# Performance work log

Measured on AMD Instinct MI355X. Metric: run time of the kernel, lower is better.

Reference implementation:

```python
import jax, jax.numpy as jnp
import numpy as np

H = 64   # LSTM hidden size
NL = 8   # LSTM layers
B, T = 2048, 64


def setup_inputs() -> dict:
    key = jax.random.key(0)
    ks = jax.random.split(key, 18)
    r = lambda i, shape, s=0.1: jax.random.normal(ks[i], shape, dtype=jnp.float32) * s
    return {
        "x": r(0, (B, T, 2), 1.0),
        "w1": r(1, (16, 2)), "b1": r(2, (16,)),
        "w2": r(3, (16, 16)), "b2": r(4, (16,)),
        "w_ih0": r(5, (4 * H, 16)), "w_hh0": r(6, (4 * H, H)),
        "b_ih0": r(7, (4 * H,)), "b_hh0": r(8, (4 * H,)),
        "w_ih": r(9, (NL - 1, 4 * H, H)), "w_hh": r(10, (NL - 1, 4 * H, H)),
        "b_ih": r(11, (NL - 1, 4 * H)), "b_hh": r(12, (NL - 1, 4 * H)),
        "wo1": r(13, (32, H)), "bo1": r(14, (32,)),
        "wo2": r(15, (4, 32)), "bo2": r(16, (4,)),
    }


def _lstm_layer(x, w_ih, w_hh, b):
    # x: [B, T, I]; torch gate order: i, f, g, o
    bsz = x.shape[0]
    xg = jnp.einsum('bti,gi->btg', x, w_ih) + b  # [B, T, 4H] precomputed input gates

    def step(carry, xg_t):
        h, c = carry
        gates = xg_t + h @ w_hh.T
        i, f, g, o = jnp.split(gates, 4, axis=-1)
        i = jax.nn.sigmoid(i); f = jax.nn.sigmoid(f)
        g = jnp.tanh(g); o = jax.nn.sigmoid(o)
        c = f * c + i * g
        h = o * jnp.tanh(c)
        return (h, c), h

    h0 = jnp.zeros((bsz, H), x.dtype)
    _, hs = jax.lax.scan(step, (h0, h0), jnp.swapaxes(xg, 0, 1))  # [T, B, H]
    return jnp.swapaxes(hs, 0, 1)


def reference(x, w1, b1, w2, b2, w_ih0, w_hh0, b_ih0, b_hh0,
              w_ih, w_hh, b_ih, b_hh, wo1, bo1, wo2, bo2):
    # action-input MLP: 2 -> 16 -> relu -> 16
    h = jax.nn.relu(x @ w1.T + b1) @ w2.T + b2
    # 8-layer LSTM, hidden 64
    h = _lstm_layer(h, w_ih0, w_hh0, b_ih0 + b_hh0)
    for l in range(NL - 1):
        h = _lstm_layer(h, w_ih[l], w_hh[l], b_ih[l] + b_hh[l])
    # output MLP: 64 -> 32 -> relu -> 4
    return jax.nn.relu(h @ wo1.T + bo1) @ wo2.T + bo2
```

## Files before the change

### kernel.cpp

```cpp
#include <hip/hip_runtime.h>


#define BATCH 2048
#define TT 64
#define HH 64
#define RS 72

typedef short bf16x8 __attribute__((ext_vector_type(8)));
typedef float f32x4 __attribute__((ext_vector_type(4)));

__device__ __forceinline__ float sigmoid_fast(float x) {
    return __builtin_amdgcn_rcpf(1.f + __expf(-x));
}
__device__ __forceinline__ float tanh_fast(float x) {
    float e = __expf(-2.f * x);
    e = fminf(e, 1e30f);
    return (1.f - e) * __builtin_amdgcn_rcpf(1.f + e);
}
__device__ __forceinline__ void split2(float x, unsigned short& hi, unsigned short& lo) {
    const unsigned u = __float_as_uint(x);
    hi = (unsigned short)(u >> 16);
    const float r = x - __uint_as_float(u & 0xFFFF0000u);
    lo = (unsigned short)(__float_as_uint(r) >> 16);
}
__device__ __forceinline__ unsigned short bf16_rne(float x) {
    const unsigned u = __float_as_uint(x);
    return (unsigned short)((u + 0x7FFFu + ((u >> 16) & 1u)) >> 16);
}
__device__ __forceinline__ void wg_wait(int* c, int v) {
    while (__hip_atomic_load(c, __ATOMIC_ACQUIRE, __HIP_MEMORY_SCOPE_WORKGROUP) < v) {}
}
__device__ __forceinline__ void wg_bump(int* c, int lane) {
    if (lane == 0)
        __hip_atomic_fetch_add(c, 1, __ATOMIC_RELEASE, __HIP_MEMORY_SCOPE_WORKGROUP);
}

__global__ __launch_bounds__(256)
void mlp_in_kernel(const float* __restrict__ x,
                   const float* __restrict__ w1, const float* __restrict__ b1,
                   const float* __restrict__ w2, const float* __restrict__ b2,
                   float* __restrict__ out) {
    const int gid = blockIdx.x * 256 + threadIdx.x;
    const float x0 = x[gid * 2 + 0];
    const float x1 = x[gid * 2 + 1];
    float hid[16];
#pragma unroll
    for (int j = 0; j < 16; ++j) {
        float v = fmaf(x1, w1[j * 2 + 1], fmaf(x0, w1[j * 2 + 0], b1[j]));
        hid[j] = fmaxf(0.f, v);
    }
    float o[16];
#pragma unroll
    for (int oo = 0; oo < 16; ++oo) {
        float acc = b2[oo];
#pragma unroll
        for (int j = 0; j < 16; ++j) acc = fmaf(hid[j], w2[oo * 16 + j], acc);
        o[oo] = acc;
    }
    float4* op = (float4*)(out + gid * 16);
#pragma unroll
    for (int q = 0; q < 4; ++q) {
        float4 v;
        v.x = o[q * 4 + 0]; v.y = o[q * 4 + 1]; v.z = o[q * 4 + 2]; v.w = o[q * 4 + 3];
        op[q] = v;
    }
}

template <int IA, int IPADA>
__global__ __launch_bounds__(512, 2)
void lstm_pair(const float* __restrict__ xmlp,
               unsigned* __restrict__ P,
               float* __restrict__ houtf,
               const int last,
               const float* __restrict__ wihA, const float* __restrict__ whhA,
               const float* __restrict__ biA, const float* __restrict__ bhA,
               const float* __restrict__ wihB, const float* __restrict__ whhB,
               const float* __restrict__ biB, const float* __restrict__ bhB) {
    constexpr int KTA = (IPADA + 64) / 32;
    constexpr int KTX = IPADA / 32;
    constexpr int LDPA = IPADA + 8;
    __shared__ __align__(16) unsigned short pAh[2][16 * LDPA], pAl[2][16 * LDPA];
    __shared__ __align__(16) unsigned short rHh[4][16 * RS], rHl[4][16 * RS];
    __shared__ __align__(16) unsigned short pHh[2][16 * RS], pHl[2][16 * RS];
    __shared__ int cA, cB, cBm;

    const int tid = threadIdx.x;
    const int wv = tid >> 6, lane = tid & 63, l16 = lane & 15, quad = lane >> 4;
    const int grp = wv >> 2;
    const int wg = wv & 3;
    const int base = blockIdx.x * 8;
    const bool lo32 = (lane < 32);
    const int bpi = (lane & 31) << 2;

    if (tid == 0) { cA = 0; cB = 0; cBm = 0; }
    for (int e = tid; e < 2 * 16 * LDPA; e += 512) { (&pAh[0][0])[e] = 0; (&pAl[0][0])[e] = 0; }
    for (int e = tid; e < 4 * 16 * RS; e += 512)   { (&rHh[0][0])[e] = 0; (&rHl[0][0])[e] = 0; }
    for (int e = tid; e < 2 * 16 * RS; e += 512)   { (&pHh[0][0])[e] = 0; (&pHl[0][0])[e] = 0; }

    const int I    = grp ? 64 : IA;
    const int IPAD = grp ? 64 : IPADA;
    const int KT   = grp ? 4  : KTA;
    const float* wih = grp ? wihB : wihA;
    const float* whh = grp ? whhB : whhA;
    const float* bi  = grp ? biB  : biA;
    const float* bh  = grp ? bhB  : bhA;

    const int jg = 16 * wg + l16;
    bf16x8 bhi[4][4];
    float bsum[4];
#pragma unroll
    for (int gt = 0; gt < 4; ++gt) {
        const int n = gt * 64 + jg;
        bsum[gt] = bi[n] + bh[n];
#pragma unroll
        for (int kt = 0; kt < 4; ++kt) {
            bf16x8 vh = {0, 0, 0, 0, 0, 0, 0, 0};
            if (kt < KT) {
#pragma unroll
                for (int j = 0; j < 8; ++j) {
                    const int k = kt * 32 + quad * 8 + j;
                    float w = 0.f;
                    if (k < I) w = wih[n * I + k];
                    else if (k >= IPAD) w = whh[n * 64 + (k - IPAD)];
                    vh[j] = (short)bf16_rne(w);
                }
            }
            bhi[kt][gt] = vh;
        }
    }

    float cs[2] = {0.f, 0.f};
    const int row0 = (quad & 1) * 4 + ((quad >> 1) << 1);

    float2 xr2 = {0.f, 0.f};
    uint2 xru = {0u, 0u};
    int sr = 0, sc = 0, srd = 0;
    bool stg = false;
    if (grp == 0) {
        if (IA == 16) {
            stg = (tid < 128);
            sr = tid >> 3; sc = (tid & 7) * 2;
            srd = base + (sr & 7);
            if (stg) {
                xr2 = *(const float2*)&xmlp[((size_t)srd * TT + 0) * 16 + sc];
                unsigned short h0, l0, h1, l1;
                split2(xr2.x, h0, l0); split2(xr2.y, h1, l1);
                *(unsigned*)&pAh[0][sr * LDPA + sc] = ((unsigned)h1 << 16) | h0;
                *(unsigned*)&pAl[0][sr * LDPA + sc] = ((unsigned)l1 << 16) | l0;
                xr2 = *(const float2*)&xmlp[((size_t)srd * TT + 1) * 16 + sc];
            }
        } else {
            stg = true;
            sr = tid >> 5; sc = (tid & 31) * 2;
            srd = base + sr;
            xru = *(const uint2*)&P[((size_t)srd * TT + 0) * 64 + sc];
            *(unsigned*)&pAh[0][sr * LDPA + sc] = (xru.y & 0xFFFF0000u) | (xru.x >> 16);
            *(unsigned*)&pAl[0][sr * LDPA + sc] = (xru.y << 16) | (xru.x & 0xFFFFu);
            xru = *(const uint2*)&P[((size_t)srd * TT + 1) * 64 + sc];
        }
    }
    __syncthreads();

    if (grp == 0) {
        __builtin_amdgcn_s_setprio(1);
        for (int t = 0; t < TT; ++t) {
            const int pb = t & 1;
            const int rsl = t & 3;
            const int rpr = (t + 3) & 3;
            if (t) wg_wait(&cA, 4 * t);
            if (stg) {
                if (IA == 16) {
                    unsigned short h0, l0, h1, l1;
                    split2(xr2.x, h0, l0); split2(xr2.y, h1, l1);
                    *(unsigned*)&pAh[pb ^ 1][sr * LDPA + sc] = ((unsigned)h1 << 16) | h0;
                    *(unsigned*)&pAl[pb ^ 1][sr * LDPA + sc] = ((unsigned)l1 << 16) | l0;
                    const int tp = (t + 2) & (TT - 1);
                    xr2 = *(const float2*)&xmlp[((size_t)srd * TT + tp) * 16 + sc];
                } else {
                    *(unsigned*)&pAh[pb ^ 1][sr * LDPA + sc] = (xru.y & 0xFFFF0000u) | (xru.x >> 16);
                    *(unsigned*)&pAl[pb ^ 1][sr * LDPA + sc] = (xru.y << 16) | (xru.x & 0xFFFFu);
                    const int tp = (t + 2) & (TT - 1);
                    xru = *(const uint2*)&P[((size_t)srd * TT + tp) * 64 + sc];
                }
            }
            bf16x8 ahi[4], alo[4];
#pragma unroll
            for (int kt = 0; kt < KTA; ++kt) {
                if (kt < KTX) {
                    const int aoff = l16 * LDPA + kt * 32 + quad * 8;
                    ahi[kt] = *(const bf16x8*)&pAh[pb][aoff];
                    alo[kt] = *(const bf16x8*)&pAl[pb][aoff];
                } else {
                    const int aoff = l16 * RS + (kt - KTX) * 32 + quad * 8;
                    ahi[kt] = *(const bf16x8*)&rHh[rpr][aoff];
                    alo[kt] = *(const bf16x8*)&rHl[rpr][aoff];
                }
            }
            f32x4 a0[4], a1[4];
#pragma unroll
            for (int gt = 0; gt < 4; ++gt) {
                a0[gt][0] = bsum[gt]; a0[gt][1] = bsum[gt];
                a0[gt][2] = bsum[gt]; a0[gt][3] = bsum[gt];
                a1[gt] = (f32x4){0.f, 0.f, 0.f, 0.f};
            }
            __builtin_amdgcn_s_setprio(2);
#pragma unroll
            for (int kt = 0; kt < KTA; ++kt) {
#pragma unroll
                for (int gt = 0; gt < 4; ++gt) {
                    a0[gt] = __builtin_amdgcn_mfma_f32_16x16x32_bf16(ahi[kt], bhi[kt][gt], a0[gt], 0, 0, 0);
                    a1[gt] = __builtin_amdgcn_mfma_f32_16x16x32_bf16(alo[kt], bhi[kt][gt], a1[gt], 0, 0, 0);
                }
            }
            __builtin_amdgcn_s_setprio(1);
            f32x4 s4[4];
#pragma unroll
            for (int gt = 0; gt < 4; ++gt) s4[gt] = a0[gt] + a1[gt];
            float gk[4][2];
#pragma unroll
            for (int gt = 0; gt < 4; ++gt) {
#pragma unroll
                for (int r = 0; r < 2; ++r) {
                    const float up = __uint_as_float(
                        __builtin_amdgcn_ds_bpermute(bpi, __float_as_uint(s4[gt][r + 2])));
                    gk[gt][r] = lo32 ? s4[gt][r] : up;
                }
            }
            float hv[2];
#pragma unroll
            for (int r = 0; r < 2; ++r) {
                const float iv = sigmoid_fast(gk[0][r]);
                const float fv = sigmoid_fast(gk[1][r]);
                const float gv = tanh_fast(gk[2][r]);
                const float ov = sigmoid_fast(gk[3][r]);
                const float cn = fv * cs[r] + iv * gv;
                cs[r] = cn;
                hv[r] = ov * tanh_fast(cn);
            }
            if (t >= 4) wg_wait(&cBm, 4 * (t - 3));
#pragma unroll
            for (int r = 0; r < 2; ++r) {
                const int R = row0 + r;
                unsigned short h_, l_;
                split2(hv[r], h_, l_);
                rHh[rsl][R * RS + jg] = h_;
                rHl[rsl][R * RS + jg] = l_;
            }
            wg_bump(&cA, lane);
        }
    } else {
        for (int t = 0; t < TT; ++t) {
            const int pb = t & 1;
            const int rsl = t & 3;
            if (t) wg_wait(&cB, 4 * t);
            wg_wait(&cA, 4 * (t + 1));
            bf16x8 ahi[4], alo[4];
#pragma unroll
            for (int kt = 0; kt < 2; ++kt) {
                const int aoff = l16 * RS + kt * 32 + quad * 8;
                ahi[kt] = *(const bf16x8*)&rHh[rsl][aoff];
                alo[kt] = *(const bf16x8*)&rHl[rsl][aoff];
            }
#pragma unroll
            for (int kt = 2; kt < 4; ++kt) {
                const int aoff = l16 * RS + (kt - 2) * 32 + quad * 8;
                ahi[kt] = *(const bf16x8*)&pHh[pb ^ 1][aoff];
                alo[kt] = *(const bf16x8*)&pHl[pb ^ 1][aoff];
            }
            wg_bump(&cBm, lane);
            f32x4 a0[4], a1[4];
#pragma unroll
            for (int gt = 0; gt < 4; ++gt) {
                a0[gt][0] = bsum[gt]; a0[gt][1] = bsum[gt];
                a0[gt][2] = bsum[gt]; a0[gt][3] = bsum[gt];
                a1[gt] = (f32x4){0.f, 0.f, 0.f, 0.f};
            }
            __builtin_amdgcn_s_setprio(1);
#pragma unroll
            for (int kt = 0; kt < 4; ++kt) {
#pragma unroll
                for (int gt = 0; gt < 4; ++gt) {
                    a0[gt] = __builtin_amdgcn_mfma_f32_16x16x32_bf16(ahi[kt], bhi[kt][gt], a0[gt], 0, 0, 0);
                    a1[gt] = __builtin_amdgcn_mfma_f32_16x16x32_bf16(alo[kt], bhi[kt][gt], a1[gt], 0, 0, 0);
                }
            }
            __builtin_amdgcn_s_setprio(0);
            f32x4 s4[4];
#pragma unroll
            for (int gt = 0; gt < 4; ++gt) s4[gt] = a0[gt] + a1[gt];
            float gk[4][2];
#pragma unroll
            for (int gt = 0; gt < 4; ++gt) {
#pragma unroll
                for (int r = 0; r < 2; ++r) {
                    const float up = __uint_as_float(
                        __builtin_amdgcn_ds_bpermute(bpi, __float_as_uint(s4[gt][r + 2])));
                    gk[gt][r] = lo32 ? s4[gt][r] : up;
                }
            }
#pragma unroll
            for (int r = 0; r < 2; ++r) {
                const float iv = sigmoid_fast(gk[0][r]);
                const float fv = sigmoid_fast(gk[1][r]);
                const float gv = tanh_fast(gk[2][r]);
                const float ov = sigmoid_fast(gk[3][r]);
                const float cn = fv * cs[r] + iv * gv;
                cs[r] = cn;
                const float h = ov * tanh_fast(cn);
                const int R = row0 + r;
                unsigned short h_, l_;
                split2(h, h_, l_);
                pHh[pb][R * RS + jg] = h_;
                pHl[pb][R * RS + jg] = l_;
                if (!last) {
                    P[((size_t)(base + R) * TT + t) * 64 + jg] =
                        ((unsigned)h_ << 16) | (unsigned)l_;
                } else {
                    houtf[((size_t)(base + R) * TT + t) * HH + jg] = h;
                }
            }
            wg_bump(&cB, lane);
        }
    }
}

__global__ __launch_bounds__(256)
void mlp_out_kernel(const float* __restrict__ hin,
                    const float* __restrict__ wo1, const float* __restrict__ bo1,
                    const float* __restrict__ wo2, const float* __restrict__ bo2,
                    float* __restrict__ out) {
    __shared__ __align__(16) float wo1_s[32 * 64];
    __shared__ float bo1_s[32];
    __shared__ float wo2_s[4 * 32];
    __shared__ float bo2_s[4];
    const int tid = threadIdx.x;
    for (int e = tid; e < 32 * 64; e += 256) wo1_s[e] = wo1[e];
    if (tid < 32) bo1_s[tid] = bo1[tid];
    if (tid < 128) wo2_s[tid] = wo2[tid];
    if (tid < 4) bo2_s[tid] = bo2[tid];
    __syncthreads();

    const int gid = blockIdx.x * 256 + tid;
    const float4* hv = (const float4*)(hin + gid * 64);
    float4 h[16];
#pragma unroll
    for (int q = 0; q < 16; ++q) h[q] = hv[q];

    float m1[32];
#pragma unroll
    for (int o = 0; o < 32; ++o) {
        float acc = bo1_s[o];
        const float4* wrow = (const float4*)(wo1_s + o * 64);
#pragma unroll
        for (int q = 0; q < 16; ++q) {
            const float4 w = wrow[q];
            acc = fmaf(h[q].x, w.x, acc);
            acc = fmaf(h[q].y, w.y, acc);
            acc = fmaf(h[q].z, w.z, acc);
            acc = fmaf(h[q].w, w.w, acc);
        }
        m1[o] = fmaxf(0.f, acc);
    }
    float r[4];
#pragma unroll
    for (int q = 0; q < 4; ++q) {
        float acc = bo2_s[q];
#pragma unroll
        for (int o = 0; o < 32; ++o) acc = fmaf(m1[o], wo2_s[q * 32 + o], acc);
        r[q] = acc;
    }
    float4 res;
    res.x = r[0]; res.y = r[1]; res.z = r[2]; res.w = r[3];
    ((float4*)out)[gid] = res;
}

extern "C" void kernel_launch(void* const* d_in, const int* in_sizes, int n_in,
                              void* d_out, int out_size, void* d_ws, size_t ws_size,
                              hipStream_t stream) {
    const float* x     = (const float*)d_in[0];
    const float* w1    = (const float*)d_in[1];
    const float* b1    = (const float*)d_in[2];
    const float* w2    = (const float*)d_in[3];
    const float* b2    = (const float*)d_in[4];
    const float* w_ih0 = (const float*)d_in[5];
    const float* w_hh0 = (const float*)d_in[6];
    const float* b_ih0 = (const float*)d_in[7];
    const float* b_hh0 = (const float*)d_in[8];
    const float* w_ih  = (const float*)d_in[9];
    const float* w_hh  = (const float*)d_in[10];
    const float* b_ih  = (const float*)d_in[11];
    const float* b_hh  = (const float*)d_in[12];
    const float* wo1   = (const float*)d_in[13];
    const float* bo1   = (const float*)d_in[14];
    const float* wo2   = (const float*)d_in[15];
    const float* bo2   = (const float*)d_in[16];

    float* buf_mlp = (float*)d_ws;
    unsigned* P = (unsigned*)(buf_mlp + (size_t)BATCH * TT * 16);
    float* bufH = (float*)(P + (size_t)BATCH * TT * 64);

    const int nbt_blocks = (BATCH * TT) / 256;

    mlp_in_kernel<<<nbt_blocks, 256, 0, stream>>>(x, w1, b1, w2, b2, buf_mlp);

    lstm_pair<16, 32><<<BATCH / 8, 512, 0, stream>>>(
        buf_mlp, P, bufH, 0,
        w_ih0, w_hh0, b_ih0, b_hh0,
        w_ih + (size_t)0 * 256 * 64, w_hh + (size_t)0 * 256 * 64, b_ih + 0 * 256, b_hh + 0 * 256);

    for (int p = 1; p < 4; ++p) {
        const int la = 2 * p - 1, lb = 2 * p;
        lstm_pair<64, 64><<<BATCH / 8, 512, 0, stream>>>(
            buf_mlp, P, bufH, (p == 3) ? 1 : 0,
            w_ih + (size_t)la * 256 * 64, w_hh + (size_t)la * 256 * 64,
            b_ih + la * 256, b_hh + la * 256,
            w_ih + (size_t)lb * 256 * 64, w_hh + (size_t)lb * 256 * 64,
            b_ih + lb * 256, b_hh + lb * 256);
    }

    mlp_out_kernel<<<nbt_blocks, 256, 0, stream>>>(bufH, wo1, bo1, wo2, bo2, (float*)d_out);
}
```

Baseline: 478.2 us.

## Fuse four LSTM layers per kernel as a wavefront pipeline across wave groups

Replaces the two-layer-per-kernel pipeline (four launches) with a four-layer-per-block pipeline using 1024-thread blocks, so the 8 layers take two launches. Each group of four waves runs one layer and hands hidden states to the next group through LDS ring buffers, synchronised by per-layer counters. This halves the global round trips of intermediate activations and the pipeline fill/drain cost. In exchange it doubles block size and LDS use, and the launch bound of 4 may limit registers and occupancy, which could serialise more work per CU.

```diff
diff --git a/kernel.cpp b/kernel.cpp
--- a/kernel.cpp
+++ b/kernel.cpp
@@ -67,43 +67,47 @@
 }
 
 template <int IA, int IPADA>
-__global__ __launch_bounds__(512, 2)
-void lstm_pair(const float* __restrict__ xmlp,
-               unsigned* __restrict__ P,
+__global__ __launch_bounds__(1024, 4)
+void lstm_quad(const float* __restrict__ xmlp,
+               const unsigned* __restrict__ Pin,
+               unsigned* __restrict__ Pout,
                float* __restrict__ houtf,
-               const int last,
-               const float* __restrict__ wihA, const float* __restrict__ whhA,
-               const float* __restrict__ biA, const float* __restrict__ bhA,
-               const float* __restrict__ wihB, const float* __restrict__ whhB,
-               const float* __restrict__ biB, const float* __restrict__ bhB) {
+               const int p0, const int last,
+               const float* __restrict__ w_ih0, const float* __restrict__ w_hh0,
+               const float* __restrict__ b_ih0, const float* __restrict__ b_hh0,
+               const float* __restrict__ w_ih, const float* __restrict__ w_hh,
+               const float* __restrict__ b_ih, const float* __restrict__ b_hh) {
     constexpr int KTA = (IPADA + 64) / 32;
     constexpr int KTX = IPADA / 32;
     constexpr int LDPA = IPADA + 8;
     __shared__ __align__(16) unsigned short pAh[2][16 * LDPA], pAl[2][16 * LDPA];
-    __shared__ __align__(16) unsigned short rHh[4][16 * RS], rHl[4][16 * RS];
+    __shared__ __align__(16) unsigned short rh[3][4][16 * RS], rl[3][4][16 * RS];
     __shared__ __align__(16) unsigned short pHh[2][16 * RS], pHl[2][16 * RS];
-    __shared__ int cA, cB, cBm;
+    __shared__ int cc[4], mm[4];
 
     const int tid = threadIdx.x;
     const int wv = tid >> 6, lane = tid & 63, l16 = lane & 15, quad = lane >> 4;
-    const int grp = wv >> 2;
+    const int l = wv >> 2;
     const int wg = wv & 3;
     const int base = blockIdx.x * 8;
     const bool lo32 = (lane < 32);
     const int bpi = (lane & 31) << 2;
 
-    if (tid == 0) { cA = 0; cB = 0; cBm = 0; }
-    for (int e = tid; e < 2 * 16 * LDPA; e += 512) { (&pAh[0][0])[e] = 0; (&pAl[0][0])[e] = 0; }
-    for (int e = tid; e < 4 * 16 * RS; e += 512)   { (&rHh[0][0])[e] = 0; (&rHl[0][0])[e] = 0; }
-    for (int e = tid; e < 2 * 16 * RS; e += 512)   { (&pHh[0][0])[e] = 0; (&pHl[0][0])[e] = 0; }
-
-    const int I    = grp ? 64 : IA;
-    const int IPAD = grp ? 64 : IPADA;
-    const int KT   = grp ? 4  : KTA;
-    const float* wih = grp ? wihB : wihA;
-    const float* whh = grp ? whhB : whhA;
-    const float* bi  = grp ? biB  : biA;
-    const float* bh  = grp ? bhB  : bhA;
+    if (tid < 4) { cc[tid] = 0; mm[tid] = 0; }
+    for (int e = tid; e < 2 * 16 * LDPA; e += 1024) { (&pAh[0][0])[e] = 0; (&pAl[0][0])[e] = 0; }
+    for (int e = tid; e < 3 * 4 * 16 * RS; e += 1024) { (&rh[0][0][0])[e] = 0; (&rl[0][0][0])[e] = 0; }
+    for (int e = tid; e < 2 * 16 * RS; e += 1024) { (&pHh[0][0])[e] = 0; (&pHl[0][0])[e] = 0; }
+
+    const int L = p0 + l;
+    const float *wih, *whh, *bi, *bh;
+    int I, IPAD, KT;
+    if (L == 0) { wih = w_ih0; whh = w_hh0; bi = b_ih0; bh = b_hh0; I = IA; IPAD = IPADA; KT = KTA; }
+    else {
+        const int li = L - 1;
+        wih = w_ih + (size_t)li * 256 * 64; whh = w_hh + (size_t)li * 256 * 64;
+        bi = b_ih + li * 256; bh = b_hh + li * 256;
+        I = 64; IPAD = 64; KT = 4;
+    }
 
     const int jg = 16 * wg + l16;
     bf16x8 bhi[4][4];
@@ -136,7 +140,7 @@
     uint2 xru = {0u, 0u};
     int sr = 0, sc = 0, srd = 0;
     bool stg = false;
-    if (grp == 0) {
+    if (l == 0 && wv < 4) {
         if (IA == 16) {
             stg = (tid < 128);
             sr = tid >> 3; sc = (tid & 7) * 2;
@@ -150,24 +154,25 @@
                 xr2 = *(const float2*)&xmlp[((size_t)srd * TT + 1) * 16 + sc];
             }
         } else {
-            stg = true;
+            stg = (tid < 256);
             sr = tid >> 5; sc = (tid & 31) * 2;
             srd = base + sr;
-            xru = *(const uint2*)&P[((size_t)srd * TT + 0) * 64 + sc];
-            *(unsigned*)&pAh[0][sr * LDPA + sc] = (xru.y & 0xFFFF0000u) | (xru.x >> 16);
-            *(unsigned*)&pAl[0][sr * LDPA + sc] = (xru.y << 16) | (xru.x & 0xFFFFu);
-            xru = *(const uint2*)&P[((size_t)srd * TT + 1) * 64 + sc];
+            if (stg) {
+                xru = *(const uint2*)&Pin[((size_t)srd * TT + 0) * 64 + sc];
+                *(unsigned*)&pAh[0][sr * LDPA + sc] = (xru.y & 0xFFFF0000u) | (xru.x >> 16);
+                *(unsigned*)&pAl[0][sr * LDPA + sc] = (xru.y << 16) | (xru.x & 0xFFFFu);
+                xru = *(const uint2*)&Pin[((size_t)srd * TT + 1) * 64 + sc];
+            }
         }
     }
     __syncthreads();
 
-    if (grp == 0) {
+    if (l == 0) {
         __builtin_amdgcn_s_setprio(1);
         for (int t = 0; t < TT; ++t) {
             const int pb = t & 1;
-            const int rsl = t & 3;
-            const int rpr = (t + 3) & 3;
-            if (t) wg_wait(&cA, 4 * t);
+            const int rsl = t & 3, rpr = (t + 3) & 3;
+            if (t) wg_wait(&cc[0], 4 * t);
             if (stg) {
                 if (IA == 16) {
                     unsigned short h0, l0, h1, l1;
@@ -180,7 +185,7 @@
                     *(unsigned*)&pAh[pb ^ 1][sr * LDPA + sc] = (xru.y & 0xFFFF0000u) | (xru.x >> 16);
                     *(unsigned*)&pAl[pb ^ 1][sr * LDPA + sc] = (xru.y << 16) | (xru.x & 0xFFFFu);
                     const int tp = (t + 2) & (TT - 1);
-                    xru = *(const uint2*)&P[((size_t)srd * TT + tp) * 64 + sc];
+                    xru = *(const uint2*)&Pin[((size_t)srd * TT + tp) * 64 + sc];
                 }
             }
             bf16x8 ahi[4], alo[4];
@@ -192,8 +197,8 @@
                     alo[kt] = *(const bf16x8*)&pAl[pb][aoff];
                 } else {
                     const int aoff = l16 * RS + (kt - KTX) * 32 + quad * 8;
-                    ahi[kt] = *(const bf16x8*)&rHh[rpr][aoff];
-                    alo[kt] = *(const bf16x8*)&rHl[rpr][aoff];
+                    ahi[kt] = *(const bf16x8*)&rh[0][rpr][aoff];
+                    alo[kt] = *(const bf16x8*)&rl[0][rpr][aoff];
                 }
             }
             f32x4 a0[4], a1[4];
@@ -237,37 +242,108 @@
                 cs[r] = cn;
                 hv[r] = ov * tanh_fast(cn);
             }
-            if (t >= 4) wg_wait(&cBm, 4 * (t - 3));
+            if (t >= 4) wg_wait(&mm[1], 4 * (t - 3));
 #pragma unroll
             for (int r = 0; r < 2; ++r) {
                 const int R = row0 + r;
                 unsigned short h_, l_;
                 split2(hv[r], h_, l_);
-                rHh[rsl][R * RS + jg] = h_;
-                rHl[rsl][R * RS + jg] = l_;
-            }
-            wg_bump(&cA, lane);
+                rh[0][rsl][R * RS + jg] = h_;
+                rl[0][rsl][R * RS + jg] = l_;
+            }
+            wg_bump(&cc[0], lane);
+        }
+    } else if (l < 3) {
+        for (int t = 0; t < TT; ++t) {
+            const int rsl = t & 3, rpr = (t + 3) & 3;
+            if (t) wg_wait(&cc[l], 4 * t);
+            wg_wait(&cc[l - 1], 4 * (t + 1));
+            bf16x8 ahi[4], alo[4];
+#pragma unroll
+            for (int kt = 0; kt < 2; ++kt) {
+                const int aoff = l16 * RS + kt * 32 + quad * 8;
+                ahi[kt] = *(const bf16x8*)&rh[l - 1][rsl][aoff];
+                alo[kt] = *(const bf16x8*)&rl[l - 1][rsl][aoff];
+            }
+            wg_bump(&mm[l], lane);
+#pragma unroll
+            for (int kt = 2; kt < 4; ++kt) {
+                const int aoff = l16 * RS + (kt - 2) * 32 + quad * 8;
+                ahi[kt] = *(const bf16x8*)&rh[l][rpr][aoff];
+                alo[kt] = *(const bf16x8*)&rl[l][rpr][aoff];
+            }
+            f32x4 a0[4], a1[4];
+#pragma unroll
+            for (int gt = 0; gt < 4; ++gt) {
+                a0[gt][0] = bsum[gt]; a0[gt][1] = bsum[gt];
+                a0[gt][2] = bsum[gt]; a0[gt][3] = bsum[gt];
+                a1[gt] = (f32x4){0.f, 0.f, 0.f, 0.f};
+            }
+            __builtin_amdgcn_s_setprio(1);
+#pragma unroll
+            for (int kt = 0; kt < 4; ++kt) {
+#pragma unroll
+                for (int gt = 0; gt < 4; ++gt) {
+                    a0[gt] = __builtin_amdgcn_mfma_f32_16x16x32_bf16(ahi[kt], bhi[kt][gt], a0[gt], 0, 0, 0);
+                    a1[gt] = __builtin_amdgcn_mfma_f32_16x16x32_bf16(alo[kt], bhi[kt][gt], a1[gt], 0, 0, 0);
+                }
+            }
+            __builtin_amdgcn_s_setprio(0);
+            f32x4 s4[4];
+#pragma unroll
+            for (int gt = 0; gt < 4; ++gt) s4[gt] = a0[gt] + a1[gt];
+            float gk[4][2];
+#pragma unroll
+            for (int gt = 0; gt < 4; ++gt) {
+#pragma unroll
+                for (int r = 0; r < 2; ++r) {
+                    const float up = __uint_as_float(
+                        __builtin_amdgcn_ds_bpermute(bpi, __float_as_uint(s4[gt][r + 2])));
+                    gk[gt][r] = lo32 ? s4[gt][r] : up;
+                }
+            }
+            float hv[2];
+#pragma unroll
+            for (int r = 0; r < 2; ++r) {
+                const float iv = sigmoid_fast(gk[0][r]);
+                const float fv = sigmoid_fast(gk[1][r]);
+                const float gv = tanh_fast(gk[2][r]);
+                const float ov = sigmoid_fast(gk[3][r]);
+                const float cn = fv * cs[r] + iv * gv;
+                cs[r] = cn;
+                hv[r] = ov * tanh_fast(cn);
+            }
+            if (t >= 4) wg_wait(&mm[l + 1], 4 * (t - 3));
+#pragma unroll
+            for (int r = 0; r < 2; ++r) {
+                const int R = row0 + r;
+                unsigned short h_, l_;
+                split2(hv[r], h_, l_);
+                rh[l][rsl][R * RS + jg] = h_;
+                rl[l][rsl][R * RS + jg] = l_;
+            }
+            wg_bump(&cc[l], lane);
         }
     } else {
         for (int t = 0; t < TT; ++t) {
             const int pb = t & 1;
             const int rsl = t & 3;
-            if (t) wg_wait(&cB, 4 * t);
-            wg_wait(&cA, 4 * (t + 1));
+            if (t) wg_wait(&cc[3], 4 * t);
+            wg_wait(&cc[2], 4 * (t + 1));
             bf16x8 ahi[4], alo[4];
 #pragma unroll
             for (int kt = 0; kt < 2; ++kt) {
                 const int aoff = l16 * RS + kt * 32 + quad * 8;
-                ahi[kt] = *(const bf16x8*)&rHh[rsl][aoff];
-                alo[kt] = *(const bf16x8*)&rHl[rsl][aoff];
-            }
+                ahi[kt] = *(const bf16x8*)&rh[2][rsl][aoff];
+                alo[kt] = *(const bf16x8*)&rl[2][rsl][aoff];
+            }
+            wg_bump(&mm[3], lane);
 #pragma unroll
             for (int kt = 2; kt < 4; ++kt) {
                 const int aoff = l16 * RS + (kt - 2) * 32 + quad * 8;
                 ahi[kt] = *(const bf16x8*)&pHh[pb ^ 1][aoff];
                 alo[kt] = *(const bf16x8*)&pHl[pb ^ 1][aoff];
             }
-            wg_bump(&cBm, lane);
             f32x4 a0[4], a1[4];
 #pragma unroll
             for (int gt = 0; gt < 4; ++gt) {
@@ -313,13 +389,13 @@
                 pHh[pb][R * RS + jg] = h_;
                 pHl[pb][R * RS + jg] = l_;
                 if (!last) {
-                    P[((size_t)(base + R) * TT + t) * 64 + jg] =
+                    Pout[((size_t)(base + R) * TT + t) * 64 + jg] =
                         ((unsigned)h_ << 16) | (unsigned)l_;
                 } else {
                     houtf[((size_t)(base + R) * TT + t) * HH + jg] = h;
                 }
             }
-            wg_bump(&cB, lane);
+            wg_bump(&cc[3], lane);
         }
     }
 }
@@ -403,20 +479,13 @@
 
     mlp_in_kernel<<<nbt_blocks, 256, 0, stream>>>(x, w1, b1, w2, b2, buf_mlp);
 
-    lstm_pair<16, 32><<<BATCH / 8, 512, 0, stream>>>(
-        buf_mlp, P, bufH, 0,
-        w_ih0, w_hh0, b_ih0, b_hh0,
-        w_ih + (size_t)0 * 256 * 64, w_hh + (size_t)0 * 256 * 64, b_ih + 0 * 256, b_hh + 0 * 256);
-
-    for (int p = 1; p < 4; ++p) {
-        const int la = 2 * p - 1, lb = 2 * p;
-        lstm_pair<64, 64><<<BATCH / 8, 512, 0, stream>>>(
-            buf_mlp, P, bufH, (p == 3) ? 1 : 0,
-            w_ih + (size_t)la * 256 * 64, w_hh + (size_t)la * 256 * 64,
-            b_ih + la * 256, b_hh + la * 256,
-            w_ih + (size_t)lb * 256 * 64, w_hh + (size_t)lb * 256 * 64,
-            b_ih + lb * 256, b_hh + lb * 256);
-    }
+    lstm_quad<16, 32><<<BATCH / 8, 1024, 0, stream>>>(
+        buf_mlp, nullptr, P, bufH, 0, 0,
+        w_ih0, w_hh0, b_ih0, b_hh0, w_ih, w_hh, b_ih, b_hh);
+
+    lstm_quad<64, 64><<<BATCH / 8, 1024, 0, stream>>>(
+        nullptr, P, nullptr, bufH, 4, 1,
+        w_ih0, w_hh0, b_ih0, b_hh0, w_ih, w_hh, b_ih, b_hh);
 
     mlp_out_kernel<<<nbt_blocks, 256, 0, stream>>>(bufH, wo1, bo1, wo2, bo2, (float*)d_out);
 }
```

Result: slower. 713.5 us (+49.2%).

## Halve batch rows per LSTM block to double grid size and occupancy

Applied to the files above, without the earlier changes.

Each lstm_pair block now handles 4 batch rows instead of 8, launching twice as many blocks, with launch bounds raised to allow 4 blocks per CU. The gate-redistribution step changes from a half-wave bpermute to a four-way bpermute select so each lane owns one row, and the staging loads are narrowed to scalars. The aim is to fill more CUs and hide the latency of the sequential recurrence. The cost is that MFMA tiles are only a quarter populated, so matrix work per useful row doubles, and register pressure is capped more tightly.

```diff
diff --git a/kernel.cpp b/kernel.cpp
--- a/kernel.cpp
+++ b/kernel.cpp
@@ -67,7 +67,7 @@
 }
 
 template <int IA, int IPADA>
-__global__ __launch_bounds__(512, 2)
+__global__ __launch_bounds__(512, 4)
 void lstm_pair(const float* __restrict__ xmlp,
                unsigned* __restrict__ P,
                float* __restrict__ houtf,
@@ -88,9 +88,8 @@
     const int wv = tid >> 6, lane = tid & 63, l16 = lane & 15, quad = lane >> 4;
     const int grp = wv >> 2;
     const int wg = wv & 3;
-    const int base = blockIdx.x * 8;
-    const bool lo32 = (lane < 32);
-    const int bpi = (lane & 31) << 2;
+    const int base = blockIdx.x * 4;
+    const int bpi4 = l16 << 2;
 
     if (tid == 0) { cA = 0; cB = 0; cBm = 0; }
     for (int e = tid; e < 2 * 16 * LDPA; e += 512) { (&pAh[0][0])[e] = 0; (&pAl[0][0])[e] = 0; }
@@ -129,34 +128,31 @@
         }
     }
 
-    float cs[2] = {0.f, 0.f};
-    const int row0 = (quad & 1) * 4 + ((quad >> 1) << 1);
-
-    float2 xr2 = {0.f, 0.f};
-    uint2 xru = {0u, 0u};
-    int sr = 0, sc = 0, srd = 0;
+    float cs = 0.f;
+
+    float xrf = 0.f;
+    unsigned xru = 0u;
+    int sr = 0, sc = 0;
     bool stg = false;
     if (grp == 0) {
         if (IA == 16) {
-            stg = (tid < 128);
-            sr = tid >> 3; sc = (tid & 7) * 2;
-            srd = base + (sr & 7);
+            stg = (tid < 64);
+            sr = tid >> 4; sc = tid & 15;
             if (stg) {
-                xr2 = *(const float2*)&xmlp[((size_t)srd * TT + 0) * 16 + sc];
-                unsigned short h0, l0, h1, l1;
-                split2(xr2.x, h0, l0); split2(xr2.y, h1, l1);
-                *(unsigned*)&pAh[0][sr * LDPA + sc] = ((unsigned)h1 << 16) | h0;
-                *(unsigned*)&pAl[0][sr * LDPA + sc] = ((unsigned)l1 << 16) | l0;
-                xr2 = *(const float2*)&xmlp[((size_t)srd * TT + 1) * 16 + sc];
+                xrf = xmlp[((size_t)(base + sr) * TT + 0) * 16 + sc];
+                unsigned short h_, l_;
+                split2(xrf, h_, l_);
+                pAh[0][sr * LDPA + sc] = h_;
+                pAl[0][sr * LDPA + sc] = l_;
+                xrf = xmlp[((size_t)(base + sr) * TT + 1) * 16 + sc];
             }
         } else {
             stg = true;
-            sr = tid >> 5; sc = (tid & 31) * 2;
-            srd = base + sr;
-            xru = *(const uint2*)&P[((size_t)srd * TT + 0) * 64 + sc];
-            *(unsigned*)&pAh[0][sr * LDPA + sc] = (xru.y & 0xFFFF0000u) | (xru.x >> 16);
-            *(unsigned*)&pAl[0][sr * LDPA + sc] = (xru.y << 16) | (xru.x & 0xFFFFu);
-            xru = *(const uint2*)&P[((size_t)srd * TT + 1) * 64 + sc];
+            sr = tid >> 6; sc = tid & 63;
+            xru = P[((size_t)(base + sr) * TT + 0) * 64 + sc];
+            pAh[0][sr * LDPA + sc] = (unsigned short)(xru >> 16);
+            pAl[0][sr * LDPA + sc] = (unsigned short)(xru & 0xFFFFu);
+            xru = P[((size_t)(base + sr) * TT + 1) * 64 + sc];
         }
     }
     __syncthreads();
@@ -170,17 +166,17 @@
             if (t) wg_wait(&cA, 4 * t);
             if (stg) {
                 if (IA == 16) {
-                    unsigned short h0, l0, h1, l1;
-                    split2(xr2.x, h0, l0); split2(xr2.y, h1, l1);
-                    *(unsigned*)&pAh[pb ^ 1][sr * LDPA + sc] = ((unsigned)h1 << 16) | h0;
-                    *(unsigned*)&pAl[pb ^ 1][sr * LDPA + sc] = ((unsigned)l1 << 16) | l0;
+                    unsigned short h_, l_;
+                    split2(xrf, h_, l_);
+                    pAh[pb ^ 1][sr * LDPA + sc] = h_;
+                    pAl[pb ^ 1][sr * LDPA + sc] = l_;
                     const int tp = (t + 2) & (TT - 1);
-                    xr2 = *(const float2*)&xmlp[((size_t)srd * TT + tp) * 16 + sc];
+                    xrf = xmlp[((size_t)(base + sr) * TT + tp) * 16 + sc];
                 } else {
-                    *(unsigned*)&pAh[pb ^ 1][sr * LDPA + sc] = (xru.y & 0xFFFF0000u) | (xru.x >> 16);
-                    *(unsigned*)&pAl[pb ^ 1][sr * LDPA + sc] = (xru.y << 16) | (xru.x & 0xFFFFu);
+                    pAh[pb ^ 1][sr * LDPA + sc] = (unsigned short)(xru >> 16);
+                    pAl[pb ^ 1][sr * LDPA + sc] = (unsigned short)(xru & 0xFFFFu);
                     const int tp = (t + 2) & (TT - 1);
-                    xru = *(const uint2*)&P[((size_t)srd * TT + tp) * 64 + sc];
+                    xru = P[((size_t)(base + sr) * TT + tp) * 64 + sc];
                 }
             }
             bf16x8 ahi[4], alo[4];
@@ -216,35 +212,28 @@
             f32x4 s4[4];
 #pragma unroll
             for (int gt = 0; gt < 4; ++gt) s4[gt] = a0[gt] + a1[gt];
-            float gk[4][2];
+            float gk[4];
 #pragma unroll
             for (int gt = 0; gt < 4; ++gt) {
-#pragma unroll
-                for (int r = 0; r < 2; ++r) {
-                    const float up = __uint_as_float(
-                        __builtin_amdgcn_ds_bpermute(bpi, __float_as_uint(s4[gt][r + 2])));
-                    gk[gt][r] = lo32 ? s4[gt][r] : up;
-                }
-            }
-            float hv[2];
-#pragma unroll
-            for (int r = 0; r < 2; ++r) {
-                const float iv = sigmoid_fast(gk[0][r]);
-                const float fv = sigmoid_fast(gk[1][r]);
-                const float gv = tanh_fast(gk[2][r]);
-                const float ov = sigmoid_fast(gk[3][r]);
-                const float cn = fv * cs[r] + iv * gv;
-                cs[r] = cn;
-                hv[r] = ov * tanh_fast(cn);
-            }
+                const float t0 = __uint_as_float(__builtin_amdgcn_ds_bpermute(bpi4, __float_as_uint(s4[gt][0])));
+                const float t1 = __uint_as_float(__builtin_amdgcn_ds_bpermute(bpi4, __float_as_uint(s4[gt][1])));
+                const float t2 = __uint_as_float(__builtin_amdgcn_ds_bpermute(bpi4, __float_as_uint(s4[gt][2])));
+                const float t3 = __uint_as_float(__builtin_amdgcn_ds_bpermute(bpi4, __float_as_uint(s4[gt][3])));
+                gk[gt] = (quad == 0) ? t0 : (quad == 1) ? t1 : (quad == 2) ? t2 : t3;
+            }
+            const float iv = sigmoid_fast(gk[0]);
+            const float fv = sigmoid_fast(gk[1]);
+            const float gv = tanh_fast(gk[2]);
+            const float ov = sigmoid_fast(gk[3]);
+            const float cn = fv * cs + iv * gv;
+            cs = cn;
+            const float hval = ov * tanh_fast(cn);
             if (t >= 4) wg_wait(&cBm, 4 * (t - 3));
-#pragma unroll
-            for (int r = 0; r < 2; ++r) {
-                const int R = row0 + r;
+            {
                 unsigned short h_, l_;
-                split2(hv[r], h_, l_);
-                rHh[rsl][R * RS + jg] = h_;
-                rHl[rsl][R * RS + jg] = l_;
+                split2(hval, h_, l_);
+                rHh[rsl][quad * RS + jg] = h_;
+                rHl[rsl][quad * RS + jg] = l_;
             }
             wg_bump(&cA, lane);
         }
@@ -288,35 +277,32 @@
             f32x4 s4[4];
 #pragma unroll
             for (int gt = 0; gt < 4; ++gt) s4[gt] = a0[gt] + a1[gt];
-            float gk[4][2];
+            float gk[4];
 #pragma unroll
             for (int gt = 0; gt < 4; ++gt) {
-#pragma unroll
-                for (int r = 0; r < 2; ++r) {
-                    const float up = __uint_as_float(
-                        __builtin_amdgcn_ds_bpermute(bpi, __float_as_uint(s4[gt][r + 2])));
-                    gk[gt][r] = lo32 ? s4[gt][r] : up;
-                }
-            }
-#pragma unroll
-            for (int r = 0; r < 2; ++r) {
-                const float iv = sigmoid_fast(gk[0][r]);
-                const float fv = sigmoid_fast(gk[1][r]);
-                const float gv = tanh_fast(gk[2][r]);
-                const float ov = sigmoid_fast(gk[3][r]);
-                const float cn = fv * cs[r] + iv * gv;
-                cs[r] = cn;
-                const float h = ov * tanh_fast(cn);
-                const int R = row0 + r;
+                const float t0 = __uint_as_float(__builtin_amdgcn_ds_bpermute(bpi4, __float_as_uint(s4[gt][0])));
+                const float t1 = __uint_as_float(__builtin_amdgcn_ds_bpermute(bpi4, __float_as_uint(s4[gt][1])));
+                const float t2 = __uint_as_float(__builtin_amdgcn_ds_bpermute(bpi4, __float_as_uint(s4[gt][2])));
+                const float t3 = __uint_as_float(__builtin_amdgcn_ds_bpermute(bpi4, __float_as_uint(s4[gt][3])));
+                gk[gt] = (quad == 0) ? t0 : (quad == 1) ? t1 : (quad == 2) ? t2 : t3;
+            }
+            const float iv = sigmoid_fast(gk[0]);
+            const float fv = sigmoid_fast(gk[1]);
+            const float gv = tanh_fast(gk[2]);
+            const float ov = sigmoid_fast(gk[3]);
+            const float cn = fv * cs + iv * gv;
+            cs = cn;
+            const float hval = ov * tanh_fast(cn);
+            {
                 unsigned short h_, l_;
-                split2(h, h_, l_);
-                pHh[pb][R * RS + jg] = h_;
-                pHl[pb][R * RS + jg] = l_;
+                split2(hval, h_, l_);
+                pHh[pb][quad * RS + jg] = h_;
+                pHl[pb][quad * RS + jg] = l_;
                 if (!last) {
-                    P[((size_t)(base + R) * TT + t) * 64 + jg] =
+                    P[((size_t)(base + quad) * TT + t) * 64 + jg] =
                         ((unsigned)h_ << 16) | (unsigned)l_;
                 } else {
-                    houtf[((size_t)(base + R) * TT + t) * HH + jg] = h;
+                    houtf[((size_t)(base + quad) * TT + t) * HH + jg] = hval;
                 }
             }
             wg_bump(&cB, lane);
@@ -403,14 +389,14 @@
 
     mlp_in_kernel<<<nbt_blocks, 256, 0, stream>>>(x, w1, b1, w2, b2, buf_mlp);
 
-    lstm_pair<16, 32><<<BATCH / 8, 512, 0, stream>>>(
+    lstm_pair<16, 32><<<BATCH / 4, 512, 0, stream>>>(
         buf_mlp, P, bufH, 0,
         w_ih0, w_hh0, b_ih0, b_hh0,
         w_ih + (size_t)0 * 256 * 64, w_hh + (size_t)0 * 256 * 64, b_ih + 0 * 256, b_hh + 0 * 256);
 
     for (int p = 1; p < 4; ++p) {
         const int la = 2 * p - 1, lb = 2 * p;
-        lstm_pair<64, 64><<<BATCH / 8, 512, 0, stream>>>(
+        lstm_pair<64, 64><<<BATCH / 4, 512, 0, stream>>>(
             buf_mlp, P, bufH, (p == 3) ? 1 : 0,
             w_ih + (size_t)la * 256 * 64, w_hh + (size_t)la * 256 * 64,
             b_ih + la * 256, b_hh + la * 256,
```

Result: slower. 846.8 us (+77.1%).
